# Optimization experiments

Hardware: AMD Instinct MI355X
Metric: run time of the kernel (lower is better)

The kernel has to match this reference:

```python
import jax, jax.numpy as jnp
import numpy as np

HIDDEN = 2048
N_HEADS = 16
N_KV_HEADS = 4
HEAD_DIM = HIDDEN // N_HEADS  # 128
N_GROUPS = N_HEADS // N_KV_HEADS  # 4
ROPE_BASE = 10000.0


def rope_cos_sin(seq_len, dim, dtype=jnp.float32):
    inv_freq = 1.0 / (ROPE_BASE ** (jnp.arange(0, dim, 2, dtype=jnp.float32) / dim))
    t = jnp.arange(seq_len, dtype=jnp.float32)
    freqs = jnp.einsum('i,j->ij', t, inv_freq)          # [S, dim/2]
    emb = jnp.concatenate([freqs, freqs], axis=-1)       # [S, dim]
    return emb.astype(dtype).cos(), emb.astype(dtype).sin() if False else (jnp.cos(emb).astype(dtype), jnp.sin(emb).astype(dtype))[1] and None or (jnp.cos(emb).astype(dtype), jnp.sin(emb).astype(dtype))


def _rope_tables(seq_len, dim):
    inv_freq = 1.0 / (ROPE_BASE ** (jnp.arange(0, dim, 2, dtype=jnp.float32) / dim))
    t = jnp.arange(seq_len, dtype=jnp.float32)
    freqs = jnp.einsum('i,j->ij', t, inv_freq)
    emb = jnp.concatenate([freqs, freqs], axis=-1)
    return jnp.cos(emb), jnp.sin(emb)  # each [S, dim]


def rotate_half(x):
    d = x.shape[-1] // 2
    return jnp.concatenate([-x[..., d:], x[..., :d]], axis=-1)


def setup_inputs() -> dict:
    key = jax.random.key(0)
    ks = jax.random.split(key, 5)
    B, S = 2, 2048
    std = 0.02
    return {
        'hidden_states': jax.random.normal(ks[0], (B, S, HIDDEN), jnp.float32),
        'wq': jax.random.normal(ks[1], (HIDDEN, N_HEADS * HEAD_DIM), jnp.float32) * std,
        'wk': jax.random.normal(ks[2], (HIDDEN, N_KV_HEADS * HEAD_DIM), jnp.float32) * std,
        'wv': jax.random.normal(ks[3], (HIDDEN, N_KV_HEADS * HEAD_DIM), jnp.float32) * std,
        'wo': jax.random.normal(ks[4], (HIDDEN, HIDDEN), jnp.float32) * std,
    }


def reference(hidden_states, wq, wk, wv, wo):
    B, S, _ = hidden_states.shape
    q = (hidden_states @ wq).reshape(B, S, N_HEADS, HEAD_DIM)       # [B,S,Hq,D]
    k = (hidden_states @ wk).reshape(B, S, N_KV_HEADS, HEAD_DIM)    # [B,S,Hk,D]
    v = (hidden_states @ wv).reshape(B, S, N_KV_HEADS, HEAD_DIM)

    cos, sin = _rope_tables(S, HEAD_DIM)                            # [S,D]
    cos = cos[None, :, None, :]
    sin = sin[None, :, None, :]
    q = q * cos + rotate_half(q) * sin
    k = k * cos + rotate_half(k) * sin

    # GQA: repeat KV heads so kv head h maps to query heads h*G..h*G+G-1
    # (matches einops repeat 'b h s d -> b (h g) s d')
    k = jnp.repeat(k, N_GROUPS, axis=2)                              # [B,S,Hq,D]
    v = jnp.repeat(v, N_GROUPS, axis=2)

    scale = 1.0 / jnp.sqrt(jnp.asarray(HEAD_DIM, q.dtype))
    scores = jnp.einsum('bqhd,bkhd->bhqk', q, k) * scale            # [B,H,S,S]
    causal = jnp.triu(jnp.full((S, S), -jnp.inf, dtype=scores.dtype), k=1)
    scores = scores + causal
    probs = jax.nn.softmax(scores.astype(jnp.float32), axis=-1).astype(q.dtype)
    out = jnp.einsum('bhqk,bkhd->bqhd', probs, v)                   # [B,S,H,D]
    out = out.reshape(B, S, HIDDEN)
    return out @ wo
```

## Files before the change

kernel.cpp:

```cpp
#include <hip/hip_runtime.h>

#define HIDDEN 2048
#define NH 16
#define NKV 4
#define HD 128
#define BATCH 2
#define SEQ 2048
#define MROWS (BATCH*SEQ)
#define NQKV (NH*HD + 2*NKV*HD)
#define KOFF (NH*HD)
#define VOFF (NH*HD + NKV*HD)

typedef unsigned short u16;
typedef unsigned int u32;
typedef __bf16 bf16_t;
typedef bf16_t bf16x8 __attribute__((ext_vector_type(8)));
typedef float f32x4 __attribute__((ext_vector_type(4)));
typedef u16 u16x8 __attribute__((ext_vector_type(8)));

__device__ __forceinline__ u16 f2bf(float f) {
  return __builtin_bit_cast(u16, (__bf16)f);
}
__device__ __forceinline__ float bf2f(u16 h) {
  u32 u = ((u32)h) << 16;
  return __builtin_bit_cast(float, u);
}

__global__ void cast_f32_bf16(const float* __restrict__ in, u16* __restrict__ out, int n8) {
  int i = blockIdx.x * blockDim.x + threadIdx.x;
  if (i >= n8) return;
  const float4* p = (const float4*)in + (size_t)i * 2;
  float4 a = p[0], b = p[1];
  u16x8 o;
  o[0]=f2bf(a.x); o[1]=f2bf(a.y); o[2]=f2bf(a.z); o[3]=f2bf(a.w);
  o[4]=f2bf(b.x); o[5]=f2bf(b.y); o[6]=f2bf(b.z); o[7]=f2bf(b.w);
  *((u16x8*)out + i) = o;
}

__global__ void transpose_cast(const float* __restrict__ src, u16* __restrict__ dst, int K, int N) {
  __shared__ float tile[32][33];
  int k0 = blockIdx.y * 32, n0 = blockIdx.x * 32;
  int tx = threadIdx.x, ty = threadIdx.y;
  #pragma unroll
  for (int j = 0; j < 32; j += 8)
    tile[ty + j][tx] = src[(size_t)(k0 + ty + j) * N + n0 + tx];
  __syncthreads();
  #pragma unroll
  for (int j = 0; j < 32; j += 8)
    dst[(size_t)(n0 + ty + j) * K + k0 + tx] = f2bf(tile[tx][ty + j]);
}

template<int OUT_BF16>
__global__ __launch_bounds__(512, 2) void gemm256(const u16* __restrict__ A, const u16* __restrict__ Bt,
                                                  void* __restrict__ Cout, int M, int N, int K) {
  __shared__ u16 As[2][256 * 64];
  __shared__ u16 Bs[2][256 * 64];
  const int tid = threadIdx.x;
  const int lane = tid & 63, wave = tid >> 6;
  const int mb = blockIdx.y * 256, nb = blockIdx.x * 256;
  const int wm = (wave >> 2) * 128;
  const int wn = (wave & 3) * 64;
  const int NT = K >> 6;

  const int rsub = tid >> 3;
  const int scol = (tid & 7) ^ (rsub & 7);
  const int wbase = (tid & ~63);

  auto stage = [&](int buf, int kt) {
    #pragma unroll
    for (int j = 0; j < 4; ++j) {
      int r = j * 64 + rsub;
      const u16* ga = A + (size_t)(mb + r) * K + kt * 64 + scol * 8;
      __builtin_amdgcn_global_load_lds((const __attribute__((address_space(1))) u32*)ga,
          (__attribute__((address_space(3))) u32*)&As[buf][(j * 512 + wbase) * 8], 16, 0, 0);
      const u16* gb = Bt + (size_t)(nb + r) * K + kt * 64 + scol * 8;
      __builtin_amdgcn_global_load_lds((const __attribute__((address_space(1))) u32*)gb,
          (__attribute__((address_space(3))) u32*)&Bs[buf][(j * 512 + wbase) * 8], 16, 0, 0);
    }
  };

  f32x4 acc[8][4];
  #pragma unroll
  for (int i = 0; i < 8; ++i)
    #pragma unroll
    for (int j = 0; j < 4; ++j) acc[i][j] = (f32x4)0.0f;

  const int arow = (lane & 15) * 64;
  const int axor = lane & 7;
  const int asel = lane >> 4;

  stage(0, 0);
  __syncthreads();
  for (int i = 0; i < NT; ++i) {
    int cur = i & 1;
    if (i + 1 < NT) stage(cur ^ 1, i + 1);

    bf16x8 af[4][2], bfr[2][2];
    #pragma unroll
    for (int mi = 0; mi < 4; ++mi)
      #pragma unroll
      for (int ks = 0; ks < 2; ++ks)
        af[mi][ks] = __builtin_bit_cast(bf16x8,
          *(const u16x8*)&As[cur][(wm + mi * 16) * 64 + arow + (((ks * 4 + asel)) ^ axor) * 8]);
    #pragma unroll
    for (int ni = 0; ni < 2; ++ni)
      #pragma unroll
      for (int ks = 0; ks < 2; ++ks)
        bfr[ni][ks] = __builtin_bit_cast(bf16x8,
          *(const u16x8*)&Bs[cur][(wn + ni * 16) * 64 + arow + (((ks * 4 + asel)) ^ axor) * 8]);
    __builtin_amdgcn_s_setprio(1);
    #pragma unroll
    for (int mi = 0; mi < 4; ++mi)
      #pragma unroll
      for (int ni = 0; ni < 2; ++ni)
        #pragma unroll
        for (int ks = 0; ks < 2; ++ks)
          acc[mi][ni] = __builtin_amdgcn_mfma_f32_16x16x32_bf16(af[mi][ks], bfr[ni][ks], acc[mi][ni], 0, 0, 0);
    __builtin_amdgcn_s_setprio(0);
    #pragma unroll
    for (int ni = 0; ni < 2; ++ni)
      #pragma unroll
      for (int ks = 0; ks < 2; ++ks)
        bfr[ni][ks] = __builtin_bit_cast(bf16x8,
          *(const u16x8*)&Bs[cur][(wn + (2 + ni) * 16) * 64 + arow + (((ks * 4 + asel)) ^ axor) * 8]);
    __builtin_amdgcn_s_setprio(1);
    #pragma unroll
    for (int mi = 0; mi < 4; ++mi)
      #pragma unroll
      for (int ni = 0; ni < 2; ++ni)
        #pragma unroll
        for (int ks = 0; ks < 2; ++ks)
          acc[mi][2 + ni] = __builtin_amdgcn_mfma_f32_16x16x32_bf16(af[mi][ks], bfr[ni][ks], acc[mi][2 + ni], 0, 0, 0);
    __builtin_amdgcn_s_setprio(0);
    #pragma unroll
    for (int mi = 0; mi < 4; ++mi)
      #pragma unroll
      for (int ks = 0; ks < 2; ++ks)
        af[mi][ks] = __builtin_bit_cast(bf16x8,
          *(const u16x8*)&As[cur][(wm + (4 + mi) * 16) * 64 + arow + (((ks * 4 + asel)) ^ axor) * 8]);
    __builtin_amdgcn_s_setprio(1);
    #pragma unroll
    for (int mi = 0; mi < 4; ++mi)
      #pragma unroll
      for (int ni = 0; ni < 2; ++ni)
        #pragma unroll
        for (int ks = 0; ks < 2; ++ks)
          acc[4 + mi][2 + ni] = __builtin_amdgcn_mfma_f32_16x16x32_bf16(af[mi][ks], bfr[ni][ks], acc[4 + mi][2 + ni], 0, 0, 0);
    __builtin_amdgcn_s_setprio(0);
    #pragma unroll
    for (int ni = 0; ni < 2; ++ni)
      #pragma unroll
      for (int ks = 0; ks < 2; ++ks)
        bfr[ni][ks] = __builtin_bit_cast(bf16x8,
          *(const u16x8*)&Bs[cur][(wn + ni * 16) * 64 + arow + (((ks * 4 + asel)) ^ axor) * 8]);
    __builtin_amdgcn_s_setprio(1);
    #pragma unroll
    for (int mi = 0; mi < 4; ++mi)
      #pragma unroll
      for (int ni = 0; ni < 2; ++ni)
        #pragma unroll
        for (int ks = 0; ks < 2; ++ks)
          acc[4 + mi][ni] = __builtin_amdgcn_mfma_f32_16x16x32_bf16(af[mi][ks], bfr[ni][ks], acc[4 + mi][ni], 0, 0, 0);
    __builtin_amdgcn_s_setprio(0);

    __syncthreads();
  }
  int rbase = mb + wm + (lane >> 4) * 4;
  int cbase = nb + wn + (lane & 15);
  #pragma unroll
  for (int mi = 0; mi < 8; ++mi) {
    #pragma unroll
    for (int r = 0; r < 4; ++r) {
      int row = rbase + mi * 16 + r;
      #pragma unroll
      for (int ni = 0; ni < 4; ++ni) {
        int col = cbase + ni * 16;
        float v = acc[mi][ni][r];
        if (OUT_BF16) ((u16*)Cout)[(size_t)row * N + col] = f2bf(v);
        else          ((float*)Cout)[(size_t)row * N + col] = v;
      }
    }
  }
}

__global__ void rope_kernel(u16* __restrict__ qkv) {
  int idx = blockIdx.x * blockDim.x + threadIdx.x;
  int d = idx & 63;
  int t = idx >> 6;
  int hd = t % 20;
  int row = t / 20;
  int s = row & (SEQ - 1);
  int cb = (hd < NH) ? hd * HD : KOFF + (hd - NH) * HD;
  float inv = __expf((float)d * -0.14391156f);
  float freq = (float)s * inv;
  float sn = sinf(freq), cs = cosf(freq);
  size_t base = (size_t)row * NQKV + cb + d;
  float x0 = bf2f(qkv[base]), x1 = bf2f(qkv[base + 64]);
  qkv[base]      = f2bf(x0 * cs - x1 * sn);
  qkv[base + 64] = f2bf(x1 * cs + x0 * sn);
}

__global__ void vtrans_kernel(const u16* __restrict__ qkv, u16* __restrict__ vt) {
  __shared__ u16 tile[32][33];
  int bh = blockIdx.z;
  int d0 = blockIdx.y * 32;
  int s0 = blockIdx.x * 32;
  int b = bh >> 2, kvh = bh & 3;
  int tx = threadIdx.x, ty = threadIdx.y;
  const u16* src = qkv + (size_t)(b * SEQ) * NQKV + VOFF + kvh * HD;
  #pragma unroll
  for (int j = 0; j < 32; j += 8)
    tile[ty + j][tx] = src[(size_t)(s0 + ty + j) * NQKV + d0 + tx];
  __syncthreads();
  u16* dst = vt + (size_t)bh * HD * SEQ;
  #pragma unroll
  for (int j = 0; j < 32; j += 8)
    dst[(size_t)(d0 + ty + j) * SEQ + s0 + tx] = tile[tx][ty + j];
}

__global__ __launch_bounds__(256, 2) void attn_kernel(const u16* __restrict__ qkv,
                                                      const u16* __restrict__ vt,
                                                      u16* __restrict__ out) {
  __shared__ u16 Ks[2][64 * 128];
  __shared__ u16 Vs[2][128 * 64];
  __shared__ u16 Ps[4][16 * 64];
  const int tid = threadIdx.x, lane = tid & 63, wave = tid >> 6;
  const int qtA = blockIdx.x, qtB = 31 - qtA;
  const int h = blockIdx.y, b = blockIdx.z;
  const int kvh = h >> 2;
  const int q0A = qtA * 64 + wave * 16;
  const int q0B = qtB * 64 + wave * 16;
  const float scale2 = 0.12751743f;

  const u16* kbase = qkv + (size_t)(b * SEQ) * NQKV + KOFF + kvh * HD;
  const u16* vbase = vt + (size_t)(b * NKV + kvh) * HD * SEQ;

  bf16x8 qfA[4], qfB[4];
  {
    const u16* qa = qkv + (size_t)(b * SEQ + q0A + (lane & 15)) * NQKV + h * HD + (lane >> 4) * 8;
    const u16* qb = qkv + (size_t)(b * SEQ + q0B + (lane & 15)) * NQKV + h * HD + (lane >> 4) * 8;
    #pragma unroll
    for (int kc = 0; kc < 4; ++kc) {
      qfA[kc] = __builtin_bit_cast(bf16x8, *(const u16x8*)(qa + kc * 32));
      qfB[kc] = __builtin_bit_cast(bf16x8, *(const u16x8*)(qb + kc * 32));
    }
  }
  f32x4 oaccA[8], oaccB[8];
  float mA[4], lA[4], mB[4], lB[4];
  #pragma unroll
  for (int i = 0; i < 8; ++i) { oaccA[i] = (f32x4)0.0f; oaccB[i] = (f32x4)0.0f; }
  #pragma unroll
  for (int r = 0; r < 4; ++r) { mA[r] = -INFINITY; lA[r] = 0.0f; mB[r] = -INFINITY; lB[r] = 0.0f; }

  const int krow = tid >> 4;
  const int kslot = (tid & 15) ^ (krow & 7);
  const int vrow = tid >> 3;
  const int vslot = (tid & 7) ^ (vrow & 7);
  const int wbase = (tid & ~63);

  auto stage = [&](int buf, int t) {
    int kv0 = t * 64;
    #pragma unroll
    for (int j = 0; j < 4; ++j) {
      const u16* src = kbase + (size_t)(kv0 + j * 16 + krow) * NQKV + kslot * 8;
      __builtin_amdgcn_global_load_lds((const __attribute__((address_space(1))) u32*)src,
          (__attribute__((address_space(3))) u32*)&Ks[buf][(j * 256 + wbase) * 8], 16, 0, 0);
    }
    #pragma unroll
    for (int j = 0; j < 4; ++j) {
      const u16* src = vbase + (size_t)(j * 32 + vrow) * SEQ + kv0 + vslot * 8;
      __builtin_amdgcn_global_load_lds((const __attribute__((address_space(1))) u32*)src,
          (__attribute__((address_space(3))) u32*)&Vs[buf][(j * 256 + wbase) * 8], 16, 0, 0);
    }
  };

  auto do_ctx = [&](const bf16x8 (&qf)[4], f32x4 (&oacc)[8], float (&mr)[4], float (&lr)[4],
                    int q0c, int kv0, int cur) {
    f32x4 sacc[4];
    #pragma unroll
    for (int n2 = 0; n2 < 4; ++n2) sacc[n2] = (f32x4)0.0f;
    #pragma unroll
    for (int n2 = 0; n2 < 4; ++n2) {
      int kvr = n2 * 16 + (lane & 15);
      #pragma unroll
      for (int kc = 0; kc < 4; ++kc) {
        int ch = (kc * 4 + (lane >> 4)) ^ (kvr & 7);
        bf16x8 kf = __builtin_bit_cast(bf16x8, *(const u16x8*)&Ks[cur][kvr * 128 + ch * 8]);
        sacc[n2] = __builtin_amdgcn_mfma_f32_16x16x32_bf16(qf[kc], kf, sacc[n2], 0, 0, 0);
      }
    }
    const bool full = (kv0 + 63 <= q0c);
    u16* pwb = &Ps[wave][0];
    #pragma unroll
    for (int r = 0; r < 4; ++r) {
      int qr = (lane >> 4) * 4 + r;
      float p0, p1, p2, p3;
      if (full) {
        p0 = sacc[0][r] * scale2; p1 = sacc[1][r] * scale2;
        p2 = sacc[2][r] * scale2; p3 = sacc[3][r] * scale2;
      } else {
        int q = q0c + qr;
        int kvc = kv0 + (lane & 15);
        p0 = (kvc       <= q) ? sacc[0][r] * scale2 : -INFINITY;
        p1 = (kvc + 16  <= q) ? sacc[1][r] * scale2 : -INFINITY;
        p2 = (kvc + 32  <= q) ? sacc[2][r] * scale2 : -INFINITY;
        p3 = (kvc + 48  <= q) ? sacc[3][r] * scale2 : -INFINITY;
      }
      float v = fmaxf(fmaxf(p0, p1), fmaxf(p2, p3));
      v = fmaxf(v, __shfl_xor(v, 1));
      v = fmaxf(v, __shfl_xor(v, 2));
      v = fmaxf(v, __shfl_xor(v, 4));
      v = fmaxf(v, __shfl_xor(v, 8));
      float m = mr[r];
      if (v > m + 8.0f) {
        float corr = exp2f(m - v);
        lr[r] *= corr;
        #pragma unroll
        for (int nt = 0; nt < 8; ++nt) oacc[nt][r] *= corr;
        m = v; mr[r] = v;
      }
      float e0 = exp2f(p0 - m), e1 = exp2f(p1 - m);
      float e2 = exp2f(p2 - m), e3 = exp2f(p3 - m);
      float ps = (e0 + e1) + (e2 + e3);
      ps += __shfl_xor(ps, 1);
      ps += __shfl_xor(ps, 2);
      ps += __shfl_xor(ps, 4);
      ps += __shfl_xor(ps, 8);
      lr[r] += ps;
      char* base = (char*)pwb + qr * 128 + (lane & 7) * 2;
      int half = (lane & 15) >> 3;
      *(u16*)(base + (((0 + half) ^ (qr & 7)) << 4)) = f2bf(e0);
      *(u16*)(base + (((2 + half) ^ (qr & 7)) << 4)) = f2bf(e1);
      *(u16*)(base + (((4 + half) ^ (qr & 7)) << 4)) = f2bf(e2);
      *(u16*)(base + (((6 + half) ^ (qr & 7)) << 4)) = f2bf(e3);
    }
    asm volatile("s_waitcnt lgkmcnt(0)" ::: "memory");
    bf16x8 pf[2];
    #pragma unroll
    for (int k2 = 0; k2 < 2; ++k2) {
      int q = lane & 15;
      int ch = (k2 * 4 + (lane >> 4)) ^ (q & 7);
      pf[k2] = __builtin_bit_cast(bf16x8, *(const u16x8*)((const char*)pwb + q * 128 + ch * 16));
    }
    #pragma unroll
    for (int nt = 0; nt < 8; ++nt) {
      int d = nt * 16 + (lane & 15);
      #pragma unroll
      for (int k2 = 0; k2 < 2; ++k2) {
        int ch = (k2 * 4 + (lane >> 4)) ^ (d & 7);
        bf16x8 vf = __builtin_bit_cast(bf16x8, *(const u16x8*)&Vs[cur][d * 64 + ch * 8]);
        oacc[nt] = __builtin_amdgcn_mfma_f32_16x16x32_bf16(pf[k2], vf, oacc[nt], 0, 0, 0);
      }
    }
  };

  const int nt_tiles = qtB + 1;
  stage(0, 0);
  __syncthreads();
  for (int t = 0; t < nt_tiles; ++t) {
    int cur = t & 1;
    if (t + 1 < nt_tiles) stage(cur ^ 1, t + 1);
    int kv0 = t * 64;
    if (kv0 <= q0A + 15) do_ctx(qfA, oaccA, mA, lA, q0A, kv0, cur);
    if (kv0 <= q0B + 15) do_ctx(qfB, oaccB, mB, lB, q0B, kv0, cur);
    __syncthreads();
  }
  #pragma unroll
  for (int r = 0; r < 4; ++r) {
    float invA = 1.0f / lA[r], invB = 1.0f / lB[r];
    #pragma unroll
    for (int nt = 0; nt < 8; ++nt) {
      int col = h * HD + nt * 16 + (lane & 15);
      int rowA = b * SEQ + q0A + (lane >> 4) * 4 + r;
      int rowB = b * SEQ + q0B + (lane >> 4) * 4 + r;
      out[(size_t)rowA * HIDDEN + col] = f2bf(oaccA[nt][r] * invA);
      out[(size_t)rowB * HIDDEN + col] = f2bf(oaccB[nt][r] * invB);
    }
  }
}

extern "C" void kernel_launch(void* const* d_in, const int* in_sizes, int n_in,
                              void* d_out, int out_size, void* d_ws, size_t ws_size,
                              hipStream_t stream) {
  (void)in_sizes; (void)n_in; (void)out_size; (void)ws_size;
  const float* x  = (const float*)d_in[0];
  const float* wq = (const float*)d_in[1];
  const float* wk = (const float*)d_in[2];
  const float* wv = (const float*)d_in[3];
  const float* wo = (const float*)d_in[4];
  float* out = (float*)d_out;
  char* ws = (char*)d_ws;

  u16* xbf   = (u16*)(ws);
  u16* wqkvt = (u16*)(ws + (size_t)16777216);
  u16* wot   = (u16*)(ws + (size_t)16777216 + 12582912);
  u16* qkv   = (u16*)(ws + (size_t)16777216 + 12582912 + 8388608);
  u16* vtb   = (u16*)(ws + (size_t)16777216 + 12582912 + 8388608 + 25165824);
  u16* aout  = xbf;

  cast_f32_bf16<<<4096, 256, 0, stream>>>(x, xbf, MROWS * HIDDEN / 8);
  transpose_cast<<<dim3(64, 64), dim3(32, 8), 0, stream>>>(wq, wqkvt, HIDDEN, 2048);
  transpose_cast<<<dim3(16, 64), dim3(32, 8), 0, stream>>>(wk, wqkvt + (size_t)2048 * 2048, HIDDEN, 512);
  transpose_cast<<<dim3(16, 64), dim3(32, 8), 0, stream>>>(wv, wqkvt + (size_t)2560 * 2048, HIDDEN, 512);
  transpose_cast<<<dim3(64, 64), dim3(32, 8), 0, stream>>>(wo, wot, HIDDEN, HIDDEN);

  gemm256<1><<<dim3(NQKV / 256, MROWS / 256), 512, 0, stream>>>(xbf, wqkvt, qkv, MROWS, NQKV, HIDDEN);
  rope_kernel<<<(MROWS * 20 * 64) / 256, 256, 0, stream>>>(qkv);
  vtrans_kernel<<<dim3(SEQ / 32, HD / 32, BATCH * NKV), dim3(32, 8), 0, stream>>>(qkv, vtb);
  attn_kernel<<<dim3(16, NH, BATCH), 256, 0, stream>>>(qkv, vtb, aout);
  gemm256<0><<<dim3(HIDDEN / 256, MROWS / 256), 512, 0, stream>>>(aout, wot, out, MROWS, HIDDEN, HIDDEN);
}
```

Measured before the change: 387.1 us.

## Shrink GEMM tile to 256x128 and use fine-grained vmcnt waits instead of syncthreads

The projection GEMMs switch from 256x256 block tiles to 256x128 tiles with eight waves each owning a 64x64 sub-tile, so the grid has twice as many blocks. This fills more of the CUs on the small QKV and output GEMMs. The main loop now waits on vmcnt for the current stage before a raw barrier instead of a full __syncthreads after compute, letting the next stage's loads overlap with compute. The smaller tile lowers arithmetic intensity per block and raises redundant A-tile loads.

```diff
diff --git a/kernel.cpp b/kernel.cpp
--- a/kernel.cpp
+++ b/kernel.cpp
@@ -51,20 +51,20 @@
 }
 
 template<int OUT_BF16>
-__global__ __launch_bounds__(512, 2) void gemm256(const u16* __restrict__ A, const u16* __restrict__ Bt,
-                                                  void* __restrict__ Cout, int M, int N, int K) {
+__global__ __launch_bounds__(512) void gemm8p(const u16* __restrict__ A, const u16* __restrict__ Bt,
+                                              void* __restrict__ Cout, int M, int N, int K) {
   __shared__ u16 As[2][256 * 64];
-  __shared__ u16 Bs[2][256 * 64];
+  __shared__ u16 Bs[2][128 * 64];
   const int tid = threadIdx.x;
   const int lane = tid & 63, wave = tid >> 6;
-  const int mb = blockIdx.y * 256, nb = blockIdx.x * 256;
-  const int wm = (wave >> 2) * 128;
-  const int wn = (wave & 3) * 64;
+  const int mb = blockIdx.y * 256, nb = blockIdx.x * 128;
+  const int wm = (wave >> 1) * 64;
+  const int wn = (wave & 1) * 64;
   const int NT = K >> 6;
 
   const int rsub = tid >> 3;
   const int scol = (tid & 7) ^ (rsub & 7);
-  const int wbase = (tid & ~63);
+  const int wbase = tid & ~63;
 
   auto stage = [&](int buf, int kt) {
     #pragma unroll
@@ -73,102 +73,76 @@
       const u16* ga = A + (size_t)(mb + r) * K + kt * 64 + scol * 8;
       __builtin_amdgcn_global_load_lds((const __attribute__((address_space(1))) u32*)ga,
           (__attribute__((address_space(3))) u32*)&As[buf][(j * 512 + wbase) * 8], 16, 0, 0);
+    }
+    #pragma unroll
+    for (int j = 0; j < 2; ++j) {
+      int r = j * 64 + rsub;
       const u16* gb = Bt + (size_t)(nb + r) * K + kt * 64 + scol * 8;
       __builtin_amdgcn_global_load_lds((const __attribute__((address_space(1))) u32*)gb,
           (__attribute__((address_space(3))) u32*)&Bs[buf][(j * 512 + wbase) * 8], 16, 0, 0);
     }
   };
 
-  f32x4 acc[8][4];
-  #pragma unroll
-  for (int i = 0; i < 8; ++i)
+  f32x4 acc[4][4];
+  #pragma unroll
+  for (int i = 0; i < 4; ++i)
     #pragma unroll
     for (int j = 0; j < 4; ++j) acc[i][j] = (f32x4)0.0f;
 
-  const int arow = (lane & 15) * 64;
-  const int axor = lane & 7;
-  const int asel = lane >> 4;
+  const int frow = lane & 15;
+  const int fhi = lane >> 4;
 
   stage(0, 0);
   __syncthreads();
-  for (int i = 0; i < NT; ++i) {
-    int cur = i & 1;
-    if (i + 1 < NT) stage(cur ^ 1, i + 1);
-
-    bf16x8 af[4][2], bfr[2][2];
-    #pragma unroll
-    for (int mi = 0; mi < 4; ++mi)
-      #pragma unroll
-      for (int ks = 0; ks < 2; ++ks)
-        af[mi][ks] = __builtin_bit_cast(bf16x8,
-          *(const u16x8*)&As[cur][(wm + mi * 16) * 64 + arow + (((ks * 4 + asel)) ^ axor) * 8]);
-    #pragma unroll
-    for (int ni = 0; ni < 2; ++ni)
-      #pragma unroll
-      for (int ks = 0; ks < 2; ++ks)
-        bfr[ni][ks] = __builtin_bit_cast(bf16x8,
-          *(const u16x8*)&Bs[cur][(wn + ni * 16) * 64 + arow + (((ks * 4 + asel)) ^ axor) * 8]);
-    __builtin_amdgcn_s_setprio(1);
-    #pragma unroll
-    for (int mi = 0; mi < 4; ++mi)
-      #pragma unroll
-      for (int ni = 0; ni < 2; ++ni)
+
+  for (int t = 0; t < NT; ++t) {
+    int cur = t & 1;
+    if (t + 1 < NT) {
+      stage(cur ^ 1, t + 1);
+      asm volatile("s_waitcnt vmcnt(6)" ::: "memory");
+    } else {
+      asm volatile("s_waitcnt vmcnt(0)" ::: "memory");
+    }
+    __builtin_amdgcn_s_barrier();
+
+    bf16x8 bfr[4][2];
+    #pragma unroll
+    for (int ni = 0; ni < 4; ++ni)
+      #pragma unroll
+      for (int kk = 0; kk < 2; ++kk) {
+        int row = wn + ni * 16 + frow;
+        int ch = (kk * 4 + fhi) ^ (row & 7);
+        bfr[ni][kk] = __builtin_bit_cast(bf16x8, *(const u16x8*)&Bs[cur][row * 64 + ch * 8]);
+      }
+    #pragma unroll
+    for (int ph = 0; ph < 2; ++ph) {
+      bf16x8 af[2][2];
+      #pragma unroll
+      for (int mi = 0; mi < 2; ++mi)
         #pragma unroll
-        for (int ks = 0; ks < 2; ++ks)
-          acc[mi][ni] = __builtin_amdgcn_mfma_f32_16x16x32_bf16(af[mi][ks], bfr[ni][ks], acc[mi][ni], 0, 0, 0);
-    __builtin_amdgcn_s_setprio(0);
-    #pragma unroll
-    for (int ni = 0; ni < 2; ++ni)
-      #pragma unroll
-      for (int ks = 0; ks < 2; ++ks)
-        bfr[ni][ks] = __builtin_bit_cast(bf16x8,
-          *(const u16x8*)&Bs[cur][(wn + (2 + ni) * 16) * 64 + arow + (((ks * 4 + asel)) ^ axor) * 8]);
-    __builtin_amdgcn_s_setprio(1);
-    #pragma unroll
-    for (int mi = 0; mi < 4; ++mi)
-      #pragma unroll
-      for (int ni = 0; ni < 2; ++ni)
+        for (int kk = 0; kk < 2; ++kk) {
+          int row = wm + (ph * 2 + mi) * 16 + frow;
+          int ch = (kk * 4 + fhi) ^ (row & 7);
+          af[mi][kk] = __builtin_bit_cast(bf16x8, *(const u16x8*)&As[cur][row * 64 + ch * 8]);
+        }
+      __builtin_amdgcn_s_setprio(1);
+      #pragma unroll
+      for (int mi = 0; mi < 2; ++mi)
         #pragma unroll
-        for (int ks = 0; ks < 2; ++ks)
-          acc[mi][2 + ni] = __builtin_amdgcn_mfma_f32_16x16x32_bf16(af[mi][ks], bfr[ni][ks], acc[mi][2 + ni], 0, 0, 0);
-    __builtin_amdgcn_s_setprio(0);
-    #pragma unroll
-    for (int mi = 0; mi < 4; ++mi)
-      #pragma unroll
-      for (int ks = 0; ks < 2; ++ks)
-        af[mi][ks] = __builtin_bit_cast(bf16x8,
-          *(const u16x8*)&As[cur][(wm + (4 + mi) * 16) * 64 + arow + (((ks * 4 + asel)) ^ axor) * 8]);
-    __builtin_amdgcn_s_setprio(1);
-    #pragma unroll
-    for (int mi = 0; mi < 4; ++mi)
-      #pragma unroll
-      for (int ni = 0; ni < 2; ++ni)
-        #pragma unroll
-        for (int ks = 0; ks < 2; ++ks)
-          acc[4 + mi][2 + ni] = __builtin_amdgcn_mfma_f32_16x16x32_bf16(af[mi][ks], bfr[ni][ks], acc[4 + mi][2 + ni], 0, 0, 0);
-    __builtin_amdgcn_s_setprio(0);
-    #pragma unroll
-    for (int ni = 0; ni < 2; ++ni)
-      #pragma unroll
-      for (int ks = 0; ks < 2; ++ks)
-        bfr[ni][ks] = __builtin_bit_cast(bf16x8,
-          *(const u16x8*)&Bs[cur][(wn + ni * 16) * 64 + arow + (((ks * 4 + asel)) ^ axor) * 8]);
-    __builtin_amdgcn_s_setprio(1);
-    #pragma unroll
-    for (int mi = 0; mi < 4; ++mi)
-      #pragma unroll
-      for (int ni = 0; ni < 2; ++ni)
-        #pragma unroll
-        for (int ks = 0; ks < 2; ++ks)
-          acc[4 + mi][ni] = __builtin_amdgcn_mfma_f32_16x16x32_bf16(af[mi][ks], bfr[ni][ks], acc[4 + mi][ni], 0, 0, 0);
-    __builtin_amdgcn_s_setprio(0);
-
-    __syncthreads();
-  }
-  int rbase = mb + wm + (lane >> 4) * 4;
-  int cbase = nb + wn + (lane & 15);
-  #pragma unroll
-  for (int mi = 0; mi < 8; ++mi) {
+        for (int ni = 0; ni < 4; ++ni)
+          #pragma unroll
+          for (int kk = 0; kk < 2; ++kk)
+            acc[ph * 2 + mi][ni] = __builtin_amdgcn_mfma_f32_16x16x32_bf16(
+                af[mi][kk], bfr[ni][kk], acc[ph * 2 + mi][ni], 0, 0, 0);
+      __builtin_amdgcn_s_setprio(0);
+    }
+    __builtin_amdgcn_s_barrier();
+  }
+
+  int rbase = mb + wm + fhi * 4;
+  int cbase = nb + wn + frow;
+  #pragma unroll
+  for (int mi = 0; mi < 4; ++mi) {
     #pragma unroll
     for (int r = 0; r < 4; ++r) {
       int row = rbase + mi * 16 + r;
@@ -404,9 +378,9 @@
   transpose_cast<<<dim3(16, 64), dim3(32, 8), 0, stream>>>(wv, wqkvt + (size_t)2560 * 2048, HIDDEN, 512);
   transpose_cast<<<dim3(64, 64), dim3(32, 8), 0, stream>>>(wo, wot, HIDDEN, HIDDEN);
 
-  gemm256<1><<<dim3(NQKV / 256, MROWS / 256), 512, 0, stream>>>(xbf, wqkvt, qkv, MROWS, NQKV, HIDDEN);
+  gemm8p<1><<<dim3(NQKV / 128, MROWS / 256), 512, 0, stream>>>(xbf, wqkvt, qkv, MROWS, NQKV, HIDDEN);
   rope_kernel<<<(MROWS * 20 * 64) / 256, 256, 0, stream>>>(qkv);
   vtrans_kernel<<<dim3(SEQ / 32, HD / 32, BATCH * NKV), dim3(32, 8), 0, stream>>>(qkv, vtb);
   attn_kernel<<<dim3(16, NH, BATCH), 256, 0, stream>>>(qkv, vtb, aout);
-  gemm256<0><<<dim3(HIDDEN / 256, MROWS / 256), 512, 0, stream>>>(aout, wot, out, MROWS, HIDDEN, HIDDEN);
-}
+  gemm8p<0><<<dim3(HIDDEN / 128, MROWS / 256), 512, 0, stream>>>(aout, wot, out, MROWS, HIDDEN, HIDDEN);
+}
```

Result: no change. 384.9 us (-0.6%).
